# Kernel optimization log

Hardware: AMD Instinct MI355X
Metric: run time of the kernel (lower is better)

Reference implementation:

```python
import jax, jax.numpy as jnp
import numpy as np

BITS = 4
MAXQ = (1 << BITS) - 1          # 15
ELEMS = 32 // BITS              # values packed per int32
GROUPSIZE = 128
M, K, N = 4096, 4096, 11008
G = K // GROUPSIZE              # 32 groups


def dequantize(qweight, scales, qzeros, g_idx):
    """Unpack GPTQ int4 weights -> fp16 [K, N], matching matmul_248_kernel."""
    K_ = g_idx.shape[0]
    N_ = scales.shape[1]
    k = jnp.arange(K_)
    # weight: value k,n packed in qweight[k // ELEMS, n] at bit offset (k % ELEMS)*BITS
    w = (qweight[k // ELEMS] >> ((k % ELEMS) * BITS)[:, None].astype(jnp.int32)) & MAXQ  # [K, N]
    # zeros: value g,n packed in qzeros[g, n // ELEMS] at bit offset (n % ELEMS)*BITS; kernel adds +1
    n = jnp.arange(N_)
    z = ((qzeros[:, n // ELEMS] >> ((n % ELEMS) * BITS)[None, :].astype(jnp.int32)) & MAXQ) + 1  # [G, N]
    gi = g_idx.astype(jnp.int32)
    # b = (b - zeros) * scales, per-group via g_idx row mapping
    W = scales[gi] * (w - z[gi]).astype(scales.dtype)  # fp16 [K, N]
    return W


def setup_inputs() -> dict:
    key = jax.random.key(0)
    k1, k2, k3, k4 = jax.random.split(key, 4)
    x = (jax.random.normal(k1, (M, K), dtype=jnp.float32) * 0.05).astype(jnp.float16)
    imin = jnp.iinfo(jnp.int32).min
    imax = jnp.iinfo(jnp.int32).max
    qweight = jax.random.randint(k2, (K // ELEMS, N), imin, imax, dtype=jnp.int32)
    qzeros = jax.random.randint(k3, (G, N // ELEMS), imin, imax, dtype=jnp.int32)
    scales = (jax.random.uniform(k4, (G, N), dtype=jnp.float32) * 0.009 + 0.001).astype(jnp.float16)
    g_idx = (jnp.arange(K, dtype=jnp.int32) // GROUPSIZE).astype(jnp.int32)
    return {"x": x, "qweight": qweight, "scales": scales, "qzeros": qzeros, "g_idx": g_idx}


def reference(x, qweight, scales, qzeros, g_idx):
    W = dequantize(qweight, scales, qzeros, g_idx)
    # fp16 inputs, fp32 accumulation, fp16 store (as in the Triton kernel)
    out = jnp.dot(x, W, preferred_element_type=jnp.float32).astype(jnp.float16)
    return out
```

## Files before the change

kernel.cpp:

```cpp
#include <hip/hip_runtime.h>

typedef unsigned short u16;
typedef unsigned int   u32;
typedef _Float16       f16;

#define M_DIM 4096
#define K_DIM 4096
#define N_DIM 11008
#define NQ8   (N_DIM / 8)

typedef f16   f16x8 __attribute__((ext_vector_type(8)));
typedef f16   f16x2 __attribute__((ext_vector_type(2)));
typedef float f32x4 __attribute__((ext_vector_type(4)));
typedef u32   u32x4 __attribute__((ext_vector_type(4)));

typedef __attribute__((address_space(1))) void GV;
typedef __attribute__((address_space(3))) void LV;
typedef __attribute__((address_space(3))) f16   lf16;
typedef __attribute__((address_space(3))) f16x8 lf16x8;
typedef __attribute__((address_space(3))) u32x4 lu32x4;

#define BAR()    __builtin_amdgcn_s_barrier()
#define WAITV(N) asm volatile("s_waitcnt vmcnt(" #N ")" ::: "memory")
#define WAITL0() asm volatile("s_waitcnt lgkmcnt(0)" ::: "memory")

__device__ __forceinline__ u32 pk2(float lo, float hi) {
    return __builtin_bit_cast(u32, __builtin_amdgcn_cvt_pkrtz(lo, hi));
}

__global__ __launch_bounds__(256) void cvt_x(const float* __restrict__ x, f16* __restrict__ xh) {
    const size_t t = (size_t)blockIdx.x * 256 + threadIdx.x;
    const float4* p = (const float4*)(x + t * 8);
    float4 a0 = p[0], a1 = p[1];
    u32x4 v;
    v.x = pk2(a0.x, a1.x); v.y = pk2(a0.y, a1.y);
    v.z = pk2(a0.z, a1.z); v.w = pk2(a0.w, a1.w);
    *(u32x4*)(xh + t * 8) = v;
}

__device__ __forceinline__ u32x4 dq8(u32 q, f16x2 b2, f16x2 s2) {
    u32 pk[4];
    #pragma unroll
    for (int j = 0; j < 4; j++) {
        const u32 mb = ((q >> (4 * j)) & 0x000F000Fu) | 0x64006400u;
        f16x2 v2 = __builtin_bit_cast(f16x2, mb);
        f16x2 w2 = (v2 + b2) * s2;
        pk[j] = __builtin_bit_cast(u32, w2);
    }
    u32x4 r; r.x = pk[0]; r.y = pk[1]; r.z = pk[2]; r.w = pk[3];
    return r;
}

#define BM 256
#define BN 256
#define BK 64

#define LDA(MH, BUF) do { \
    _Pragma("unroll") for (int mf = 0; mf < 4; ++mf) { \
        af[mf][0] = *(const lf16x8*)(pAr0 + (BUF)*16384 + (MH)*4096 + mf*1024); \
        af[mf][1] = *(const lf16x8*)(pAr1 + (BUF)*16384 + (MH)*4096 + mf*1024); \
    } } while (0)

#define LDB(BF, NH, BUF) do { \
    _Pragma("unroll") for (int nf = 0; nf < 2; ++nf) { \
        BF[nf][0] = *(const lf16x8*)(pBr0 + (BUF)*16384 + (NH)*2048 + nf*1024); \
        BF[nf][1] = *(const lf16x8*)(pBr1 + (BUF)*16384 + (NH)*2048 + nf*1024); \
    } } while (0)

#define STAGE_A(J, BUF, PTR) __builtin_amdgcn_global_load_lds( \
    (GV*)(PTR), (LV*)(&As[0][0] + (BUF)*16384 + (tid + (J)*512)*8), 16, 0, 0)

#define STAGE_B(R, BUF, BQ, B2, S2) \
    *(lu32x4*)(pBw + (BUF)*16384 + bwo[R]) = dq8((BQ)[R], (B2), (S2))

#define MFMA16(AI, BF, CJ) do { \
    _Pragma("unroll") for (int ks = 0; ks < 2; ++ks) \
    _Pragma("unroll") for (int mf = 0; mf < 4; ++mf) \
    _Pragma("unroll") for (int nf = 0; nf < 2; ++nf) \
        acc[(AI)+mf][(CJ)+nf] = __builtin_amdgcn_mfma_f32_16x16x32_f16( \
            af[mf][ks], (BF)[nf][ks], acc[(AI)+mf][(CJ)+nf], 0, 0, 0); \
    } while (0)

#define PRIO1() __builtin_amdgcn_s_setprio(1)
#define PRIO0() __builtin_amdgcn_s_setprio(0)

__global__ __launch_bounds__(512, 2)
void gptq_gemm_big(const f16* __restrict__ xh, const int* __restrict__ qw,
                   const float* __restrict__ sc, const int* __restrict__ qz,
                   float* __restrict__ out)
{
    __shared__ __align__(16) f16 As[2][BM * BK];
    __shared__ __align__(16) f16 Bs[2][BN * BK];

    const int tid  = threadIdx.x;
    const int lane = tid & 63;
    const int wave = tid >> 6;
    const int quad = lane >> 4;
    const int l15  = lane & 15;
    const int sw   = l15 & 7;
    const int wm   = (wave >> 2) * 128;
    const int wn   = (wave & 3) * 64;

    const int bid0 = blockIdx.y * 43 + blockIdx.x;
    const int bid  = (bid0 & 7) * 86 + (bid0 >> 3);
    const int n0 = (bid % 43) * BN;
    const int m0 = (bid / 43) * BM;

    const int cko0 = (quad ^ sw) * 8;
    const int cko1 = ((4 + quad) ^ sw) * 8;

    const lf16* pAr0 = (const lf16*)&As[0][0] + (wm + l15) * 64 + cko0;
    const lf16* pAr1 = (const lf16*)&As[0][0] + (wm + l15) * 64 + cko1;
    const lf16* pBr0 = (const lf16*)&Bs[0][0] + (wn + l15) * 64 + cko0;
    const lf16* pBr1 = (const lf16*)&Bs[0][0] + (wn + l15) * 64 + cko1;
    lf16* pBw = (lf16*)&Bs[0][0];

    const int arow = tid >> 3;
    const int acnk = (tid & 7) ^ (arow & 7);
    const f16* agp[4];
    #pragma unroll
    for (int j = 0; j < 4; ++j)
        agp[j] = xh + (size_t)(m0 + j * 64 + arow) * K_DIM + acnk * 8;

    const int bn   = tid >> 1;
    const int bsub = tid & 1;
    const int qr0  = bsub * 4;
    const int gn   = n0 + bn;
    const int zsh  = (gn & 7) * 4;
    const int*   qcol = qw + gn;
    const int*   qzp  = qz + (gn >> 3);
    const float* scp  = sc + gn;
    int bwo[4];
    #pragma unroll
    for (int i = 0; i < 4; ++i)
        bwo[i] = (bn * 8 + ((qr0 + i) ^ (bn & 7))) * 8;

    f32x4 acc[8][4];
    #pragma unroll
    for (int i = 0; i < 8; ++i)
        #pragma unroll
        for (int j = 0; j < 4; ++j)
            acc[i][j] = (f32x4){0.f, 0.f, 0.f, 0.f};

    f16x8 af[4][2], bf0[2][2], bf1[2][2];
    u32 bqA[4], bqB[4];
    u32 zq_c; float sv_c;
    u32 zq_n; float sv_n;

    {
        zq_c = (u32)qzp[0];
        sv_c = scp[0];
        u32 bq0[4];
        #pragma unroll
        for (int j = 0; j < 4; ++j) bq0[j] = (u32)qcol[(size_t)(qr0 + j) * N_DIM];
        #pragma unroll
        for (int j = 0; j < 4; ++j) STAGE_A(j, 0, agp[j]);
        #pragma unroll
        for (int j = 0; j < 4; ++j) bqA[j] = (u32)qcol[(size_t)(8 + qr0 + j) * N_DIM];
        const f16 sh = (f16)sv_c;
        const f16 bh = (f16)(-(float)(1025 + (int)((zq_c >> zsh) & 15u)));
        const f16x2 s2 = {sh, sh}, b2 = {bh, bh};
        #pragma unroll
        for (int r = 0; r < 4; ++r) STAGE_B(r, 0, bq0, b2, s2);
        WAITV(0); WAITL0();
        BAR();
    }

    #pragma unroll 1
    for (int i = 0; i < 32; ++i) {
        const f16 shc = (f16)sv_c;
        const f16 bhc = (f16)(-(float)(1025 + (int)((zq_c >> zsh) & 15u)));
        const f16x2 s2c = {shc, shc}, b2c = {bhc, bhc};
        const int t2 = (i < 31) ? 2 * i + 2 : 63;
        const int t3 = (i < 31) ? 2 * i + 3 : 63;
        const int gnx = (i < 31) ? i + 1 : 31;
        const int a5off = (i < 31) ? 128 : 64;

        LDA(0, 0);
        LDB(bf0, 0, 0);
        STAGE_A(0, 1, agp[0] + 64);
        STAGE_A(1, 1, agp[1] + 64);
        STAGE_A(2, 1, agp[2] + 64);
        STAGE_A(3, 1, agp[3] + 64);
        BAR();
        PRIO1(); MFMA16(0, bf0, 0); PRIO0();
        LDB(bf1, 1, 0);
        #pragma unroll
        for (int j = 0; j < 4; ++j) bqB[j] = (u32)qcol[(size_t)(t2 * 8 + qr0 + j) * N_DIM];
        zq_n = (u32)qzp[(size_t)gnx * NQ8];
        sv_n = scp[(size_t)gnx * N_DIM];
        STAGE_B(0, 1, bqA, b2c, s2c);
        BAR();
        PRIO1(); MFMA16(0, bf1, 2); PRIO0();
        LDA(1, 0);
        STAGE_B(1, 1, bqA, b2c, s2c);
        BAR();
        PRIO1(); MFMA16(4, bf1, 2); PRIO0();
        STAGE_B(2, 1, bqA, b2c, s2c);
        BAR();
        PRIO1(); MFMA16(4, bf0, 0); PRIO0();
        STAGE_B(3, 1, bqA, b2c, s2c);
        WAITV(6); WAITL0();
        BAR();

        const f16 shn = (f16)sv_n;
        const f16 bhn = (f16)(-(float)(1025 + (int)((zq_n >> zsh) & 15u)));
        const f16x2 s2n = {shn, shn}, b2n = {bhn, bhn};

        LDA(0, 1);
        LDB(bf0, 0, 1);
        STAGE_A(0, 0, agp[0] + a5off);
        STAGE_A(1, 0, agp[1] + a5off);
        STAGE_A(2, 0, agp[2] + a5off);
        STAGE_A(3, 0, agp[3] + a5off);
        BAR();
        PRIO1(); MFMA16(0, bf0, 0); PRIO0();
        LDB(bf1, 1, 1);
        #pragma unroll
        for (int j = 0; j < 4; ++j) bqA[j] = (u32)qcol[(size_t)(t3 * 8 + qr0 + j) * N_DIM];
        STAGE_B(0, 0, bqB, b2n, s2n);
        BAR();
        PRIO1(); MFMA16(0, bf1, 2); PRIO0();
        LDA(1, 1);
        STAGE_B(1, 0, bqB, b2n, s2n);
        BAR();
        PRIO1(); MFMA16(4, bf1, 2); PRIO0();
        STAGE_B(2, 0, bqB, b2n, s2n);
        BAR();
        PRIO1(); MFMA16(4, bf0, 0); PRIO0();
        STAGE_B(3, 0, bqB, b2n, s2n);
        WAITV(4); WAITL0();
        BAR();

        zq_c = zq_n; sv_c = sv_n;
        #pragma unroll
        for (int j = 0; j < 4; ++j) agp[j] += 128;
    }

    WAITV(0); WAITL0();

    #pragma unroll
    for (int i = 0; i < 8; ++i) {
        const int mrow = m0 + wm + i * 16 + quad * 4;
        #pragma unroll
        for (int j = 0; j < 4; ++j) {
            const int ncol = n0 + wn + j * 16 + l15;
            float* op = out + (size_t)mrow * N_DIM + ncol;
            #pragma unroll
            for (int r = 0; r < 4; ++r)
                op[(size_t)r * N_DIM] = acc[i][j][r];
        }
    }
}

__global__ __launch_bounds__(256, 2)
void gptq_gemm_f32(const float* __restrict__ x, const int* __restrict__ qw,
                   const float* __restrict__ sc, const int* __restrict__ qz,
                   float* __restrict__ out)
{
    constexpr int AK = 40;
    __shared__ __align__(16) f16 As[128 * AK];
    __shared__ __align__(16) f16 Bs[128 * 40];

    const int tid  = threadIdx.x;
    const int lane = tid & 63;
    const int wave = tid >> 6;
    const int quad = lane >> 4;
    const int l15  = lane & 15;
    const int wm   = (wave & 1) * 64;
    const int wn   = (wave >> 1) * 64;
    const int m0 = blockIdx.y * 128;
    const int n0 = blockIdx.x * 128;

    const float* agf = x + (size_t)(m0 + (tid >> 1)) * K_DIM + (tid & 1) * 16;
    f16* alf = As + (tid >> 1) * AK + (tid & 1) * 16;

    const int dn  = tid & 127;
    const int dkq = tid >> 7;
    const int gn  = n0 + dn;
    const int zsh = (gn & 7) * 4;
    const int*   qwp = qw + gn;
    const int*   qzp = qz + (gn >> 3);
    const float* scp = sc + gn;
    f16* bs0 = Bs + dn * 40 + dkq * 8;

    f32x4 acc[4][4];
    #pragma unroll
    for (int i = 0; i < 4; i++)
        #pragma unroll
        for (int j = 0; j < 4; j++)
            acc[i][j] = (f32x4){0.f, 0.f, 0.f, 0.f};

    for (int g = 0; g < K_DIM / 128; g++) {
        const u32 zq = (u32)qzp[(size_t)g * NQ8];
        const int z1 = (int)((zq >> zsh) & 15u) + 1;
        const float s = scp[(size_t)g * N_DIM];
        const f16 sh = (f16)s;
        const f16 bh = (f16)(-(float)(1024 + z1));
        const f16x2 s2 = {sh, sh}, b2 = {bh, bh};

        #pragma unroll
        for (int t = 0; t < 4; t++) {
            const int kt = g * 4 + t;
            u32x4 bv[2];
            #pragma unroll
            for (int i = 0; i < 2; i++)
                bv[i] = dq8((u32)qwp[(size_t)(4 * kt + dkq + 2 * i) * N_DIM], b2, s2);

            const float4* agp2 = (const float4*)(agf + kt * 32);
            float4 a0 = agp2[0], a1 = agp2[1], a2 = agp2[2], a3 = agp2[3];
            u32x4 av0, av1;
            av0.x = pk2(a0.x, a1.x); av0.y = pk2(a0.y, a1.y);
            av0.z = pk2(a0.z, a1.z); av0.w = pk2(a0.w, a1.w);
            av1.x = pk2(a2.x, a3.x); av1.y = pk2(a2.y, a3.y);
            av1.z = pk2(a2.z, a3.z); av1.w = pk2(a2.w, a3.w);
            *(u32x4*)(alf)     = av0;
            *(u32x4*)(alf + 8) = av1;
            *(u32x4*)(bs0)      = bv[0];
            *(u32x4*)(bs0 + 16) = bv[1];
            __syncthreads();

            f16x8 af[4], bfr[4];
            #pragma unroll
            for (int t2 = 0; t2 < 4; t2++) {
                af[t2]  = *(const f16x8*)(As + (wm + t2 * 16 + l15) * AK + quad * 8);
                bfr[t2] = *(const f16x8*)(Bs + (wn + t2 * 16 + l15) * 40 + quad * 8);
            }
            #pragma unroll
            for (int i = 0; i < 4; i++)
                #pragma unroll
                for (int j = 0; j < 4; j++)
                    acc[i][j] = __builtin_amdgcn_mfma_f32_16x16x32_f16(af[i], bfr[j], acc[i][j], 0, 0, 0);
            __syncthreads();
        }
    }

    #pragma unroll
    for (int i = 0; i < 4; i++) {
        const int mrow = m0 + wm + i * 16 + quad * 4;
        #pragma unroll
        for (int j = 0; j < 4; j++) {
            const int ncol = n0 + wn + j * 16 + l15;
            float* op = out + (size_t)mrow * N_DIM + ncol;
            #pragma unroll
            for (int r = 0; r < 4; r++)
                op[(size_t)r * N_DIM] = acc[i][j][r];
        }
    }
}

extern "C" void kernel_launch(void* const* d_in, const int* in_sizes, int n_in,
                              void* d_out, int out_size, void* d_ws, size_t ws_size,
                              hipStream_t stream) {
    const float* x  = (const float*)d_in[0];
    const int*   qw = (const int*)d_in[1];
    const float* sc = (const float*)d_in[2];
    const int*   qz = (const int*)d_in[3];
    float* out = (float*)d_out;
    f16*   xh  = (f16*)d_ws;

    const bool pre = ws_size >= (size_t)M_DIM * K_DIM * sizeof(f16);
    if (pre) {
        cvt_x<<<(M_DIM * K_DIM / 8) / 256, 256, 0, stream>>>(x, xh);
        gptq_gemm_big<<<dim3(N_DIM / BN, M_DIM / BM), 512, 0, stream>>>(xh, qw, sc, qz, out);
    } else {
        gptq_gemm_f32<<<dim3(N_DIM / 128, M_DIM / 128), 256, 0, stream>>>(x, qw, sc, qz, out);
    }
}
```

Measured before the change: 575.3 us.

## Dequantize GPTQ weights directly into MFMA register fragments, dropping B LDS staging

Each wave now loads packed int4 qweight words straight from global memory in the layout its MFMA B fragments need, and dequantizes them in registers. This removes the shared-memory B buffers and the B LDS writes and reads. It also removes most intra-iteration barriers, leaving one wait-and-barrier per half step, and halves LDS usage. In exchange, the two wave rows that share a column slice each load and dequantize the same weights. That doubles weight global loads and dequant ALU work, and the global loads are only partially coalesced (64-byte row segments per quad).

After: 722.0 us. +25.5%, slower.

```diff
diff --git a/kernel.cpp b/kernel.cpp
--- a/kernel.cpp
+++ b/kernel.cpp
@@ -18,7 +18,6 @@
 typedef __attribute__((address_space(3))) void LV;
 typedef __attribute__((address_space(3))) f16   lf16;
 typedef __attribute__((address_space(3))) f16x8 lf16x8;
-typedef __attribute__((address_space(3))) u32x4 lu32x4;
 
 #define BAR()    __builtin_amdgcn_s_barrier()
 #define WAITV(N) asm volatile("s_waitcnt vmcnt(" #N ")" ::: "memory")
@@ -38,7 +37,7 @@
     *(u32x4*)(xh + t * 8) = v;
 }
 
-__device__ __forceinline__ u32x4 dq8(u32 q, f16x2 b2, f16x2 s2) {
+__device__ __forceinline__ f16x8 dq8f(u32 q, f16x2 b2, f16x2 s2) {
     u32 pk[4];
     #pragma unroll
     for (int j = 0; j < 4; j++) {
@@ -48,7 +47,7 @@
         pk[j] = __builtin_bit_cast(u32, w2);
     }
     u32x4 r; r.x = pk[0]; r.y = pk[1]; r.z = pk[2]; r.w = pk[3];
-    return r;
+    return __builtin_bit_cast(f16x8, r);
 }
 
 #define BM 256
@@ -61,17 +60,36 @@
         af[mf][1] = *(const lf16x8*)(pAr1 + (BUF)*16384 + (MH)*4096 + mf*1024); \
     } } while (0)
 
-#define LDB(BF, NH, BUF) do { \
-    _Pragma("unroll") for (int nf = 0; nf < 2; ++nf) { \
-        BF[nf][0] = *(const lf16x8*)(pBr0 + (BUF)*16384 + (NH)*2048 + nf*1024); \
-        BF[nf][1] = *(const lf16x8*)(pBr1 + (BUF)*16384 + (NH)*2048 + nf*1024); \
-    } } while (0)
-
 #define STAGE_A(J, BUF, PTR) __builtin_amdgcn_global_load_lds( \
     (GV*)(PTR), (LV*)(&As[0][0] + (BUF)*16384 + (tid + (J)*512)*8), 16, 0, 0)
 
-#define STAGE_B(R, BUF, BQ, B2, S2) \
-    *(lu32x4*)(pBw + (BUF)*16384 + bwo[R]) = dq8((BQ)[R], (B2), (S2))
+#define LOADQ(TT) do { \
+    _Pragma("unroll") for (int j = 0; j < 4; ++j) { \
+        bq[2*j+0] = (u32)qw[(size_t)((TT)*8 +     quad) * N_DIM + ncol[j]]; \
+        bq[2*j+1] = (u32)qw[(size_t)((TT)*8 + 4 + quad) * N_DIM + ncol[j]]; \
+    } } while (0)
+
+#define LOADP(G) do { \
+    _Pragma("unroll") for (int j = 0; j < 4; ++j) { \
+        zqv[j] = (u32)qz[(size_t)(G) * NQ8 + (ncol[j] >> 3)]; \
+        svv[j] = sc[(size_t)(G) * N_DIM + ncol[j]]; \
+    } } while (0)
+
+#define CONVP() do { \
+    _Pragma("unroll") for (int j = 0; j < 4; ++j) { \
+        const int z1 = (int)((zqv[j] >> zsh) & 15u) + 1; \
+        const f16 bh = (f16)(-(float)(1024 + z1)); \
+        const f16 sh = (f16)svv[j]; \
+        b2h[j] = (f16x2){bh, bh}; s2h[j] = (f16x2){sh, sh}; \
+    } } while (0)
+
+#define DQTILE() do { \
+    _Pragma("unroll") for (int nf = 0; nf < 2; ++nf) { \
+        bf0[nf][0] = dq8f(bq[2*nf+0],     b2h[nf],   s2h[nf]); \
+        bf0[nf][1] = dq8f(bq[2*nf+1],     b2h[nf],   s2h[nf]); \
+        bf1[nf][0] = dq8f(bq[2*(2+nf)+0], b2h[2+nf], s2h[2+nf]); \
+        bf1[nf][1] = dq8f(bq[2*(2+nf)+1], b2h[2+nf], s2h[2+nf]); \
+    } } while (0)
 
 #define MFMA16(AI, BF, CJ) do { \
     _Pragma("unroll") for (int ks = 0; ks < 2; ++ks) \
@@ -90,7 +108,6 @@
                    float* __restrict__ out)
 {
     __shared__ __align__(16) f16 As[2][BM * BK];
-    __shared__ __align__(16) f16 Bs[2][BN * BK];
 
     const int tid  = threadIdx.x;
     const int lane = tid & 63;
@@ -111,9 +128,6 @@
 
     const lf16* pAr0 = (const lf16*)&As[0][0] + (wm + l15) * 64 + cko0;
     const lf16* pAr1 = (const lf16*)&As[0][0] + (wm + l15) * 64 + cko1;
-    const lf16* pBr0 = (const lf16*)&Bs[0][0] + (wn + l15) * 64 + cko0;
-    const lf16* pBr1 = (const lf16*)&Bs[0][0] + (wn + l15) * 64 + cko1;
-    lf16* pBw = (lf16*)&Bs[0][0];
 
     const int arow = tid >> 3;
     const int acnk = (tid & 7) ^ (arow & 7);
@@ -122,18 +136,11 @@
     for (int j = 0; j < 4; ++j)
         agp[j] = xh + (size_t)(m0 + j * 64 + arow) * K_DIM + acnk * 8;
 
-    const int bn   = tid >> 1;
-    const int bsub = tid & 1;
-    const int qr0  = bsub * 4;
-    const int gn   = n0 + bn;
-    const int zsh  = (gn & 7) * 4;
-    const int*   qcol = qw + gn;
-    const int*   qzp  = qz + (gn >> 3);
-    const float* scp  = sc + gn;
-    int bwo[4];
-    #pragma unroll
-    for (int i = 0; i < 4; ++i)
-        bwo[i] = (bn * 8 + ((qr0 + i) ^ (bn & 7))) * 8;
+    int ncol[4];
+    #pragma unroll
+    for (int j = 0; j < 4; ++j)
+        ncol[j] = n0 + wn + (j >> 1) * 32 + (j & 1) * 16 + l15;
+    const int zsh = (l15 & 7) * 4;
 
     f32x4 acc[8][4];
     #pragma unroll
@@ -143,96 +150,58 @@
             acc[i][j] = (f32x4){0.f, 0.f, 0.f, 0.f};
 
     f16x8 af[4][2], bf0[2][2], bf1[2][2];
-    u32 bqA[4], bqB[4];
-    u32 zq_c; float sv_c;
-    u32 zq_n; float sv_n;
+    u32 bq[8];
+    u32 zqv[4]; float svv[4];
+    f16x2 b2h[4], s2h[4];
 
     {
-        zq_c = (u32)qzp[0];
-        sv_c = scp[0];
-        u32 bq0[4];
-        #pragma unroll
-        for (int j = 0; j < 4; ++j) bq0[j] = (u32)qcol[(size_t)(qr0 + j) * N_DIM];
+        LOADP(0);
+        LOADQ(0);
         #pragma unroll
         for (int j = 0; j < 4; ++j) STAGE_A(j, 0, agp[j]);
-        #pragma unroll
-        for (int j = 0; j < 4; ++j) bqA[j] = (u32)qcol[(size_t)(8 + qr0 + j) * N_DIM];
-        const f16 sh = (f16)sv_c;
-        const f16 bh = (f16)(-(float)(1025 + (int)((zq_c >> zsh) & 15u)));
-        const f16x2 s2 = {sh, sh}, b2 = {bh, bh};
-        #pragma unroll
-        for (int r = 0; r < 4; ++r) STAGE_B(r, 0, bq0, b2, s2);
         WAITV(0); WAITL0();
         BAR();
     }
 
     #pragma unroll 1
     for (int i = 0; i < 32; ++i) {
-        const f16 shc = (f16)sv_c;
-        const f16 bhc = (f16)(-(float)(1025 + (int)((zq_c >> zsh) & 15u)));
-        const f16x2 s2c = {shc, shc}, b2c = {bhc, bhc};
-        const int t2 = (i < 31) ? 2 * i + 2 : 63;
-        const int t3 = (i < 31) ? 2 * i + 3 : 63;
-        const int gnx = (i < 31) ? i + 1 : 31;
+        const int t2   = (i < 31) ? 2 * i + 2 : 63;
+        const int gnx  = (i < 31) ? i + 1 : 31;
         const int a5off = (i < 31) ? 128 : 64;
 
+        CONVP();
+
+        DQTILE();
         LDA(0, 0);
-        LDB(bf0, 0, 0);
         STAGE_A(0, 1, agp[0] + 64);
         STAGE_A(1, 1, agp[1] + 64);
         STAGE_A(2, 1, agp[2] + 64);
         STAGE_A(3, 1, agp[3] + 64);
-        BAR();
+        LOADQ(2 * i + 1);
+        LOADP(gnx);
         PRIO1(); MFMA16(0, bf0, 0); PRIO0();
-        LDB(bf1, 1, 0);
-        #pragma unroll
-        for (int j = 0; j < 4; ++j) bqB[j] = (u32)qcol[(size_t)(t2 * 8 + qr0 + j) * N_DIM];
-        zq_n = (u32)qzp[(size_t)gnx * NQ8];
-        sv_n = scp[(size_t)gnx * N_DIM];
-        STAGE_B(0, 1, bqA, b2c, s2c);
-        BAR();
         PRIO1(); MFMA16(0, bf1, 2); PRIO0();
         LDA(1, 0);
-        STAGE_B(1, 1, bqA, b2c, s2c);
+        PRIO1(); MFMA16(4, bf1, 2); PRIO0();
+        PRIO1(); MFMA16(4, bf0, 0); PRIO0();
+        WAITV(16); WAITL0();
         BAR();
-        PRIO1(); MFMA16(4, bf1, 2); PRIO0();
-        STAGE_B(2, 1, bqA, b2c, s2c);
-        BAR();
-        PRIO1(); MFMA16(4, bf0, 0); PRIO0();
-        STAGE_B(3, 1, bqA, b2c, s2c);
-        WAITV(6); WAITL0();
-        BAR();
-
-        const f16 shn = (f16)sv_n;
-        const f16 bhn = (f16)(-(float)(1025 + (int)((zq_n >> zsh) & 15u)));
-        const f16x2 s2n = {shn, shn}, b2n = {bhn, bhn};
-
+
+        DQTILE();
         LDA(0, 1);
-        LDB(bf0, 0, 1);
         STAGE_A(0, 0, agp[0] + a5off);
         STAGE_A(1, 0, agp[1] + a5off);
         STAGE_A(2, 0, agp[2] + a5off);
         STAGE_A(3, 0, agp[3] + a5off);
-        BAR();
+        LOADQ(t2);
         PRIO1(); MFMA16(0, bf0, 0); PRIO0();
-        LDB(bf1, 1, 1);
-        #pragma unroll
-        for (int j = 0; j < 4; ++j) bqA[j] = (u32)qcol[(size_t)(t3 * 8 + qr0 + j) * N_DIM];
-        STAGE_B(0, 0, bqB, b2n, s2n);
-        BAR();
         PRIO1(); MFMA16(0, bf1, 2); PRIO0();
         LDA(1, 1);
-        STAGE_B(1, 0, bqB, b2n, s2n);
+        PRIO1(); MFMA16(4, bf1, 2); PRIO0();
+        PRIO1(); MFMA16(4, bf0, 0); PRIO0();
+        WAITV(8); WAITL0();
         BAR();
-        PRIO1(); MFMA16(4, bf1, 2); PRIO0();
-        STAGE_B(2, 0, bqB, b2n, s2n);
-        BAR();
-        PRIO1(); MFMA16(4, bf0, 0); PRIO0();
-        STAGE_B(3, 0, bqB, b2n, s2n);
-        WAITV(4); WAITL0();
-        BAR();
-
-        zq_c = zq_n; sv_c = sv_n;
+
         #pragma unroll
         for (int j = 0; j < 4; ++j) agp[j] += 128;
     }
@@ -244,13 +213,17 @@
         const int mrow = m0 + wm + i * 16 + quad * 4;
         #pragma unroll
         for (int j = 0; j < 4; ++j) {
-            const int ncol = n0 + wn + j * 16 + l15;
-            float* op = out + (size_t)mrow * N_DIM + ncol;
+            const int ncol2 = n0 + wn + j * 16 + l15;
+            float* op = out + (size_t)mrow * N_DIM + ncol2;
             #pragma unroll
             for (int r = 0; r < 4; ++r)
                 op[(size_t)r * N_DIM] = acc[i][j][r];
         }
     }
+}
+
+__device__ __forceinline__ u32x4 dq8(u32 q, f16x2 b2, f16x2 s2) {
+    return __builtin_bit_cast(u32x4, dq8f(q, b2, s2));
 }
 
 __global__ __launch_bounds__(256, 2)
```
